# Optimization experiments

Hardware: AMD Instinct MI355X
Metric: run time of the kernel (lower is better)

The kernel has to match this reference:

```python
import jax, jax.numpy as jnp
import numpy as np

N_EMBD = 1024
N_HEAD = 16
HEAD_DIM = N_EMBD // N_HEAD  # 64; scale = sqrt(64) = 8


def setup_inputs() -> dict:
    key = jax.random.key(0)
    k0, k1, k2, k3, k4 = jax.random.split(key, 5)
    B, T = 4, 2048
    x = jax.random.normal(k0, (B, T, N_EMBD), dtype=jnp.float32)
    # torch Linear weights are (out,in); we store (in,out) so y = x @ W + b
    W_attn = jax.random.normal(k1, (N_EMBD, 3 * N_EMBD), dtype=jnp.float32) * 0.02
    b_attn = jax.random.normal(k2, (3 * N_EMBD,), dtype=jnp.float32) * 0.02
    W_proj = jax.random.normal(k3, (N_EMBD, N_EMBD), dtype=jnp.float32) * 0.02
    b_proj = jax.random.normal(k4, (N_EMBD,), dtype=jnp.float32) * 0.02
    return {"x": x, "W_attn": W_attn, "b_attn": b_attn,
            "W_proj": W_proj, "b_proj": b_proj}


def reference(x, W_attn, b_attn, W_proj, b_proj):
    B, T, D = x.shape
    scale = 1.0 / np.float32(np.sqrt(HEAD_DIM))
    qkv = x @ W_attn + b_attn                      # [B,T,3D]
    q, k, v = jnp.split(qkv, 3, axis=-1)           # each [B,T,D]
    att = jnp.einsum('bid,bjd->bij', q, k) * scale # [B,T,T]
    causal = jnp.tril(jnp.ones((T, T), dtype=bool))
    att = jnp.where(causal[None, :, :], att, jnp.float32(-jnp.inf))
    att = jax.nn.softmax(att, axis=-1)
    y = jnp.einsum('bij,bjd->bid', att, v)         # [B,T,D]
    return y @ W_proj + b_proj
```

## Files before the change

### kernel.cpp

```cpp
#include <hip/hip_runtime.h>

typedef __attribute__((ext_vector_type(8))) short short8;
typedef __attribute__((ext_vector_type(4))) float f32x4;
typedef __attribute__((ext_vector_type(4))) unsigned short ushort4v;

struct DB0 { static constexpr int value = 0; };
struct DB1 { static constexpr int value = 1; };

__device__ __forceinline__ unsigned short f2bf(float f) {
  unsigned int u = __float_as_uint(f);
  u += 0x7fffu + ((u >> 16) & 1u);
  return (unsigned short)(u >> 16);
}
__device__ __forceinline__ float bf2f(unsigned short h) {
  return __uint_as_float(((unsigned int)h) << 16);
}

__device__ __forceinline__ void gload16(const unsigned short* g, unsigned short* l) {
  __builtin_amdgcn_global_load_lds(
      (const __attribute__((address_space(1))) unsigned int*)g,
      (__attribute__((address_space(3))) unsigned int*)l,
      16, 0, 0);
}

template <int OFF>
__device__ __forceinline__ short8 dsr(unsigned a) {
  short8 r;
  asm volatile("ds_read_b128 %0, %1 offset:%2" : "=v"(r) : "v"(a), "n"(OFF));
  return r;
}

__device__ __forceinline__ void bar() {
  asm volatile("" ::: "memory");
  __builtin_amdgcn_s_barrier();
  asm volatile("" ::: "memory");
}

__global__ __launch_bounds__(256) void conv_x_kernel(const float* __restrict__ x,
                                                     unsigned short* __restrict__ xb) {
  int i = blockIdx.x * 256 + threadIdx.x;
  f32x4 v = ((const f32x4*)x)[i];
  ushort4v o;
  o[0] = f2bf(v[0]); o[1] = f2bf(v[1]); o[2] = f2bf(v[2]); o[3] = f2bf(v[3]);
  ((ushort4v*)xb)[i] = o;
}

__global__ __launch_bounds__(256) void transpose_w_kernel(const float* __restrict__ W,
                                                          unsigned short* __restrict__ Wt,
                                                          int K, int N) {
  __shared__ float tile[32][33];
  int n0 = blockIdx.x * 32, k0 = blockIdx.y * 32;
  int tx = threadIdx.x, ty = threadIdx.y;
#pragma unroll
  for (int j = 0; j < 32; j += 8)
    tile[ty + j][tx] = W[(size_t)(k0 + ty + j) * N + n0 + tx];
  __syncthreads();
#pragma unroll
  for (int j = 0; j < 32; j += 8)
    Wt[(size_t)(n0 + ty + j) * K + k0 + tx] = f2bf(tile[tx][ty + j]);
}

__global__ __launch_bounds__(256) void transpose_v_kernel(const unsigned short* __restrict__ qkv,
                                                          unsigned short* __restrict__ vt) {
  __shared__ unsigned short tile[32][33];
  int b = blockIdx.z;
  int key0 = blockIdx.x * 32, d0 = blockIdx.y * 32;
  int tx = threadIdx.x, ty = threadIdx.y;
#pragma unroll
  for (int j = 0; j < 32; j += 8)
    tile[ty + j][tx] = qkv[(size_t)(b * 2048 + key0 + ty + j) * 3072 + 2048 + d0 + tx];
  __syncthreads();
#pragma unroll
  for (int j = 0; j < 32; j += 8)
    vt[(size_t)(b * 1024 + d0 + ty + j) * 2048 + key0 + tx] = tile[tx][ty + j];
}

__global__ __launch_bounds__(256) void softmax_kernel(unsigned short* __restrict__ S) {
  int row = blockIdx.x * 4 + (threadIdx.x >> 6);
  int l = threadIdx.x & 63;
  int rl = row & 2047;
  int rend = ((rl >> 7) + 1) << 7;
  unsigned short* p = S + (size_t)row * 2048;
  float v[32];
  float mx = -3e38f;
#pragma unroll
  for (int i = 0; i < 4; i++) {
    int c0 = (i * 64 + l) * 8;
    if (c0 < rend) {
      short8 raw = *(const short8*)&p[c0];
#pragma unroll
      for (int j = 0; j < 8; j++) {
        v[i * 8 + j] = bf2f((unsigned short)raw[j]);
        mx = fmaxf(mx, v[i * 8 + j]);
      }
    } else {
#pragma unroll
      for (int j = 0; j < 8; j++) v[i * 8 + j] = -3e38f;
    }
  }
#pragma unroll
  for (int off = 1; off < 64; off <<= 1) mx = fmaxf(mx, __shfl_xor(mx, off));
  float s = 0.f;
#pragma unroll
  for (int i = 0; i < 32; i++) { v[i] = exp2f((v[i] - mx) * 1.44269504f); s += v[i]; }
#pragma unroll
  for (int off = 1; off < 64; off <<= 1) s += __shfl_xor(s, off);
  float inv = 1.f / s;
#pragma unroll
  for (int i = 0; i < 4; i++) {
    int c0 = (i * 64 + l) * 8;
    if (c0 < rend) {
      short8 o;
#pragma unroll
      for (int j = 0; j < 8; j++) o[j] = (short)f2bf(v[i * 8 + j] * inv);
      *(short8*)&p[c0] = o;
    }
  }
}

template <int OUTBF>
__global__ __launch_bounds__(256) void gemm128_kernel(
    const unsigned short* __restrict__ A, int lda, long long saz,
    const unsigned short* __restrict__ Bt, int ldb, long long sbz,
    void* __restrict__ Cv, int ldc, long long scz,
    const float* __restrict__ bias, int K, float scale, int causal) {
  __shared__ __align__(16) unsigned short lds[2][16384];

  int bx, by, z;
  if (causal == 3) {
    int i = blockIdx.x;
    by = (int)((sqrtf(8.f * i + 1.f) - 1.f) * 0.5f);
    while ((by + 1) * (by + 2) / 2 <= i) by++;
    while (by * (by + 1) / 2 > i) by--;
    bx = i - by * (by + 1) / 2;
    z = blockIdx.y;
  } else if (causal == 4) {
    int gx = gridDim.x, gy = gridDim.y, gz = gridDim.z;
    int total = gx * gy * gz;
    int id = blockIdx.x + blockIdx.y * gx + blockIdx.z * gx * gy;
    int halfn = total >> 1;
    int half = id >= halfn;
    int r = id - half * halfn;
    bx = r % gx;
    int rest = r / gx;
    int by0 = rest % gy;
    z = rest / gy + half * (gz >> 1);
    by = half ? (gy - 1 - by0) : by0;
  } else {
    bx = blockIdx.x; by = blockIdx.y; z = blockIdx.z;
  }
  const int m0 = by * 128, n0 = bx * 128;
  A += (size_t)z * saz;
  Bt += (size_t)z * sbz;

  const int t = threadIdx.x;
  const int lane = t & 63, wid = t >> 6;
  const int g = lane >> 4, q = lane & 15;
  const int wm = wid >> 1, wn = wid & 1;

  int NT = K >> 6;
  if (causal == 1) { if (n0 >= m0 + 128) NT = 0; }
  else if (causal == 2 || causal == 4) { NT = min(K, m0 + 128) >> 6; }

  f32x4 acc[4][4] = {};

  if (NT > 0) {
    const int scol = ((t & 7) * 8) ^ (((t >> 3) & 7) << 3);
    const unsigned short* aS = A + (size_t)(m0 + (t >> 3)) * lda + scol;
    const unsigned short* bS = Bt + (size_t)(n0 + (t >> 3)) * ldb + scol;

    auto stage = [&](int tt) {
      unsigned short* d = &lds[tt & 1][wid * 512];
      const unsigned short* sa = aS + (size_t)tt * 64;
      const unsigned short* sb = bS + (size_t)tt * 64;
      gload16(sa, d);
      gload16(sa + (size_t)32 * lda, d + 2048);
      gload16(sa + (size_t)64 * lda, d + 4096);
      gload16(sa + (size_t)96 * lda, d + 6144);
      gload16(sb, d + 8192);
      gload16(sb + (size_t)32 * ldb, d + 10240);
      gload16(sb + (size_t)64 * ldb, d + 12288);
      gload16(sb + (size_t)96 * ldb, d + 14336);
    };

    const unsigned base =
        (unsigned)(unsigned long long)(__attribute__((address_space(3))) unsigned short*)&lds[0][0];
    const int W = (q & 7) << 4;
    const int colA0 = (g * 16) ^ W;
    const int colA1 = colA0 ^ 64;
    const unsigned aa0B = base + (unsigned)((wm * 64 + q) * 128 + colA0);
    const unsigned aa1B = base + (unsigned)((wm * 64 + q) * 128 + colA1);
    const unsigned bb0B = base + 16384u + (unsigned)((wn * 64 + q) * 128 + colA0);
    const unsigned bb1B = base + 16384u + (unsigned)((wn * 64 + q) * 128 + colA1);

    stage(0);
    asm volatile("s_waitcnt vmcnt(0)" ::: "memory");
    bar();

    auto body = [&](auto dbc, int tt) {
      constexpr int DB = decltype(dbc)::value;
      const unsigned aa0 = aa0B + DB * 32768u, aa1 = aa1B + DB * 32768u;
      const unsigned bb0 = bb0B + DB * 32768u, bb1 = bb1B + DB * 32768u;
      if (tt + 1 < NT) stage(tt + 1);
      short8 aq[4][2], bq[4][2];
      aq[0][0] = dsr<0>(aa0);    aq[0][1] = dsr<0>(aa1);
      aq[1][0] = dsr<2048>(aa0); aq[1][1] = dsr<2048>(aa1);
      aq[2][0] = dsr<4096>(aa0); aq[2][1] = dsr<4096>(aa1);
      aq[3][0] = dsr<6144>(aa0); aq[3][1] = dsr<6144>(aa1);
      bq[0][0] = dsr<0>(bb0);    bq[0][1] = dsr<0>(bb1);
      bq[1][0] = dsr<2048>(bb0); bq[1][1] = dsr<2048>(bb1);
      bq[2][0] = dsr<4096>(bb0); bq[2][1] = dsr<4096>(bb1);
      bq[3][0] = dsr<6144>(bb0); bq[3][1] = dsr<6144>(bb1);
      asm volatile("s_waitcnt lgkmcnt(0)" ::: "memory");
      __builtin_amdgcn_sched_barrier(0);
      __builtin_amdgcn_s_setprio(1);
#pragma unroll
      for (int ks = 0; ks < 2; ks++)
#pragma unroll
        for (int m = 0; m < 4; m++)
#pragma unroll
          for (int n = 0; n < 4; n++)
            acc[m][n] = __builtin_amdgcn_mfma_f32_16x16x32_bf16(aq[m][ks], bq[n][ks], acc[m][n], 0, 0, 0);
      __builtin_amdgcn_s_setprio(0);
      __builtin_amdgcn_sched_barrier(0);
      asm volatile("s_waitcnt vmcnt(0)" ::: "memory");
      bar();
    };

    int tt = 0;
    for (; tt + 2 <= NT; tt += 2) {
      body(DB0{}, tt);
      body(DB1{}, tt + 1);
    }
    if (tt < NT) body(DB0{}, tt);
  }

  const bool maskC = (causal == 1) || (causal == 3);
#pragma unroll
  for (int n = 0; n < 4; n++) {
    int colg = n0 + wn * 64 + n * 16 + q;
    float bv = bias ? bias[colg] : 0.f;
#pragma unroll
    for (int m = 0; m < 4; m++) {
      int rowb = m0 + wm * 64 + m * 16 + g * 4;
#pragma unroll
      for (int r = 0; r < 4; r++) {
        float val = acc[m][n][r] * scale + bv;
        if (maskC && colg > rowb + r) val = -1e30f;
        if (OUTBF) {
          ((unsigned short*)Cv)[(size_t)z * scz + (size_t)(rowb + r) * ldc + colg] = f2bf(val);
        } else {
          ((float*)Cv)[(size_t)z * scz + (size_t)(rowb + r) * ldc + colg] = val;
        }
      }
    }
  }
}

extern "C" void kernel_launch(void* const* d_in, const int* in_sizes, int n_in,
                              void* d_out, int out_size, void* d_ws, size_t ws_size,
                              hipStream_t stream) {
  const float* x  = (const float*)d_in[0];
  const float* Wa = (const float*)d_in[1];
  const float* ba = (const float*)d_in[2];
  const float* Wp = (const float*)d_in[3];
  const float* bp = (const float*)d_in[4];
  float* out = (float*)d_out;

  char* ws = (char*)d_ws;
  unsigned short* qkv = (unsigned short*)(ws);
  unsigned short* xb  = (unsigned short*)(ws + 50331648);
  unsigned short* vt  = (unsigned short*)(ws + 50331648);
  unsigned short* wta = (unsigned short*)(ws + 67108864);
  unsigned short* S   = (unsigned short*)(ws + 73400320);
  unsigned short* y   = (unsigned short*)(ws + 106954752);
  unsigned short* wtp = (unsigned short*)(ws + 123731968);

  conv_x_kernel<<<8192, 256, 0, stream>>>(x, xb);
  transpose_w_kernel<<<dim3(96, 32), dim3(32, 8), 0, stream>>>(Wa, wta, 1024, 3072);
  transpose_w_kernel<<<dim3(32, 32), dim3(32, 8), 0, stream>>>(Wp, wtp, 1024, 1024);

  gemm128_kernel<1><<<dim3(24, 64, 1), 256, 0, stream>>>(
      xb, 1024, 0, wta, 1024, 0, qkv, 3072, 0, ba, 1024, 1.0f, 0);

  gemm128_kernel<1><<<dim3(136, 4), 256, 0, stream>>>(
      qkv, 3072, 2048LL * 3072, qkv + 1024, 3072, 2048LL * 3072,
      S, 2048, 2048LL * 2048, nullptr, 1024, 0.125f, 3);

  softmax_kernel<<<2048, 256, 0, stream>>>(S);

  transpose_v_kernel<<<dim3(64, 32, 4), dim3(32, 8), 0, stream>>>(qkv, vt);

  gemm128_kernel<1><<<dim3(8, 16, 4), 256, 0, stream>>>(
      S, 2048, 2048LL * 2048, vt, 2048, 1024LL * 2048,
      y, 1024, 2048LL * 1024, nullptr, 2048, 1.0f, 4);

  gemm128_kernel<0><<<dim3(8, 64, 1), 256, 0, stream>>>(
      y, 1024, 0, wtp, 1024, 0, out, 1024, 0, bp, 1024, 1.0f, 0);
}
```

Measured before the change: 212.4 us.

## Fold output projection into V, deepen GEMM prefetch, add tile swizzle

```diff
diff --git a/kernel.cpp b/kernel.cpp
--- a/kernel.cpp
+++ b/kernel.cpp
@@ -58,21 +58,6 @@
 #pragma unroll
   for (int j = 0; j < 32; j += 8)
     Wt[(size_t)(n0 + ty + j) * K + k0 + tx] = f2bf(tile[tx][ty + j]);
-}
-
-__global__ __launch_bounds__(256) void transpose_v_kernel(const unsigned short* __restrict__ qkv,
-                                                          unsigned short* __restrict__ vt) {
-  __shared__ unsigned short tile[32][33];
-  int b = blockIdx.z;
-  int key0 = blockIdx.x * 32, d0 = blockIdx.y * 32;
-  int tx = threadIdx.x, ty = threadIdx.y;
-#pragma unroll
-  for (int j = 0; j < 32; j += 8)
-    tile[ty + j][tx] = qkv[(size_t)(b * 2048 + key0 + ty + j) * 3072 + 2048 + d0 + tx];
-  __syncthreads();
-#pragma unroll
-  for (int j = 0; j < 32; j += 8)
-    vt[(size_t)(b * 1024 + d0 + ty + j) * 2048 + key0 + tx] = tile[tx][ty + j];
 }
 
 __global__ __launch_bounds__(256) void softmax_kernel(unsigned short* __restrict__ S) {
@@ -148,6 +133,14 @@
     by = half ? (gy - 1 - by0) : by0;
   } else {
     bx = blockIdx.x; by = blockIdx.y; z = blockIdx.z;
+    int gx = gridDim.x, gy = gridDim.y;
+    if (causal == 0 && (gx & 7) == 0 && (gy & 7) == 0) {
+      int id = by * gx + bx;
+      int s = id >> 6, w = id & 63;
+      int spx = gx >> 3;
+      bx = (s % spx) * 8 + (w & 7);
+      by = (s / spx) * 8 + (w >> 3);
+    }
   }
   const int m0 = by * 128, n0 = bx * 128;
   A += (size_t)z * saz;
@@ -194,14 +187,18 @@
     const unsigned bb1B = base + 16384u + (unsigned)((wn * 64 + q) * 128 + colA1);
 
     stage(0);
-    asm volatile("s_waitcnt vmcnt(0)" ::: "memory");
+    if (NT > 1) {
+      stage(1);
+      asm volatile("s_waitcnt vmcnt(8)" ::: "memory");
+    } else {
+      asm volatile("s_waitcnt vmcnt(0)" ::: "memory");
+    }
     bar();
 
     auto body = [&](auto dbc, int tt) {
       constexpr int DB = decltype(dbc)::value;
       const unsigned aa0 = aa0B + DB * 32768u, aa1 = aa1B + DB * 32768u;
       const unsigned bb0 = bb0B + DB * 32768u, bb1 = bb1B + DB * 32768u;
-      if (tt + 1 < NT) stage(tt + 1);
       short8 aq[4][2], bq[4][2];
       aq[0][0] = dsr<0>(aa0);    aq[0][1] = dsr<0>(aa1);
       aq[1][0] = dsr<2048>(aa0); aq[1][1] = dsr<2048>(aa1);
@@ -213,6 +210,8 @@
       bq[3][0] = dsr<6144>(bb0); bq[3][1] = dsr<6144>(bb1);
       asm volatile("s_waitcnt lgkmcnt(0)" ::: "memory");
       __builtin_amdgcn_sched_barrier(0);
+      bar();
+      if (tt + 2 < NT) stage(tt + 2);
       __builtin_amdgcn_s_setprio(1);
 #pragma unroll
       for (int ks = 0; ks < 2; ks++)
@@ -223,7 +222,11 @@
             acc[m][n] = __builtin_amdgcn_mfma_f32_16x16x32_bf16(aq[m][ks], bq[n][ks], acc[m][n], 0, 0, 0);
       __builtin_amdgcn_s_setprio(0);
       __builtin_amdgcn_sched_barrier(0);
-      asm volatile("s_waitcnt vmcnt(0)" ::: "memory");
+      if (tt + 2 < NT) {
+        asm volatile("s_waitcnt vmcnt(8)" ::: "memory");
+      } else {
+        asm volatile("s_waitcnt vmcnt(0)" ::: "memory");
+      }
       bar();
     };
 
@@ -273,7 +276,6 @@
   unsigned short* vt  = (unsigned short*)(ws + 50331648);
   unsigned short* wta = (unsigned short*)(ws + 67108864);
   unsigned short* S   = (unsigned short*)(ws + 73400320);
-  unsigned short* y   = (unsigned short*)(ws + 106954752);
   unsigned short* wtp = (unsigned short*)(ws + 123731968);
 
   conv_x_kernel<<<8192, 256, 0, stream>>>(x, xb);
@@ -289,12 +291,11 @@
 
   softmax_kernel<<<2048, 256, 0, stream>>>(S);
 
-  transpose_v_kernel<<<dim3(64, 32, 4), dim3(32, 8), 0, stream>>>(qkv, vt);
-
-  gemm128_kernel<1><<<dim3(8, 16, 4), 256, 0, stream>>>(
-      S, 2048, 2048LL * 2048, vt, 2048, 1024LL * 2048,
-      y, 1024, 2048LL * 1024, nullptr, 2048, 1.0f, 4);
-
-  gemm128_kernel<0><<<dim3(8, 64, 1), 256, 0, stream>>>(
-      y, 1024, 0, wtp, 1024, 0, out, 1024, 0, bp, 1024, 1.0f, 0);
-}
+  gemm128_kernel<1><<<dim3(16, 8, 4), 256, 0, stream>>>(
+      wtp, 1024, 0, qkv + 2048, 3072, 2048LL * 3072,
+      vt, 2048, 2048LL * 1024, nullptr, 1024, 1.0f, 0);
+
+  gemm128_kernel<0><<<dim3(8, 16, 4), 256, 0, stream>>>(
+      S, 2048, 2048LL * 2048, vt, 2048, 2048LL * 1024,
+      out, 1024, 2048LL * 1024, bp, 2048, 1.0f, 4);
+}
```

Measured after the change: 197.8 us. -6.9%, faster.
